# Kernel optimization log

Measured on AMD Instinct MI355X. Metric: run time of the kernel, lower is better.

The kernel has to match this reference:

```python
import jax, jax.numpy as jnp
import numpy as np

S = 4          # num_residual_streams
B = 4          # batch
T = 4096       # seq_len
D = 1024       # dim
SINKHORN_ITERS = 20
EPS = 1e-05


def setup_inputs() -> dict:
    key = jax.random.key(0)
    k1, k2 = jax.random.split(key)
    residuals = jax.random.normal(k1, (B * S, T, D), dtype=jnp.float32)
    rmsnorm_weight = jnp.ones((D,), dtype=jnp.float32)
    # H_pre: -8 everywhere except layer_index % S = 0 -> 0.0
    H_pre_logits = jnp.full((S,), -8.0, dtype=jnp.float32).at[0].set(0.0)
    H_post_logits = jnp.zeros((S,), dtype=jnp.float32)
    # H_res: -8 off-diagonal, 0 on diagonal, plus alpha_init * noise
    H_res = (jnp.full((S, S), -8.0, dtype=jnp.float32) + 8.0 * jnp.eye(S, dtype=jnp.float32)
             + 0.01 * jax.random.normal(k2, (S, S), dtype=jnp.float32))
    return dict(residuals=residuals, rmsnorm_weight=rmsnorm_weight,
                H_pre_logits=H_pre_logits, H_post_logits=H_post_logits, H_res=H_res)


def _sinkhorn_knopp(M, num_iters, eps):
    # alternating row / column normalization to a doubly-stochastic matrix
    for _ in range(num_iters):
        M = M / (M.sum(axis=1, keepdims=True) + eps)
        M = M / (M.sum(axis=0, keepdims=True) + eps)
    return M


def reference(residuals, rmsnorm_weight, H_pre_logits, H_post_logits, H_res):
    s = H_pre_logits.shape[0]
    bs, t, d = residuals.shape
    b = bs // s
    # rearrange '(b s) t d -> (b t) s d'
    x = residuals.reshape(b, s, t, d).transpose(0, 2, 1, 3).reshape(b * t, s, d)
    # stream_aggregate with h_pre = sigmoid(H_pre_logits)
    h_pre = jax.nn.sigmoid(H_pre_logits)
    x_agg = jnp.einsum('nsd,s->nd', x, h_pre)
    # rmsnorm
    rms = jnp.sqrt(jnp.mean(x_agg * x_agg, axis=-1, keepdims=True) + EPS)
    x_norm = (x_agg / rms) * rmsnorm_weight
    # identity branch on the aggregated single-stream view
    branch_out = x_norm  # [(b t), d]
    # stream_distribute with h_post = 2 * sigmoid(H_post_logits)
    h_post = 2.0 * jax.nn.sigmoid(H_post_logits)
    y_dist = branch_out[:, None, :] * h_post[None, :, None]  # [(b t), s, d]
    # stream_mix with sinkhorn-normalized exp(H_res)
    M = _sinkhorn_knopp(jnp.exp(H_res), SINKHORN_ITERS, EPS)
    mixed = jnp.einsum('sr,nrd->nsd', M, y_dist)
    out = x + mixed
    # rearrange '(b t) s d -> (b s) t d'
    out = out.reshape(b, t, s, d).transpose(0, 2, 1, 3).reshape(b * s, t, d)
    return out
```

## Files before the change

kernel.cpp:

```cpp
#include <hip/hip_runtime.h>


#define S_ 4
#define T_ 4096
#define D_ 1024
#define NITER_ 20
#define EPSF_ 1e-5f

__global__ __launch_bounds__(256) void hyperconn_kernel(
    const float* __restrict__ res,
    const float* __restrict__ w,
    const float* __restrict__ hpre_l,
    const float* __restrict__ hpost_l,
    const float* __restrict__ hres,
    float* __restrict__ out)
{
    const int n   = blockIdx.x;
    const int b   = n >> 12;
    const int t   = n & (T_ - 1);
    const int tid = threadIdx.x;

    __shared__ float s_c[S_];
    __shared__ float s_part[4];

    if (tid == 0) {
        float M[S_][S_];
        #pragma unroll
        for (int i = 0; i < S_; ++i)
            #pragma unroll
            for (int j = 0; j < S_; ++j)
                M[i][j] = __expf(hres[i * S_ + j]);
        for (int it = 0; it < NITER_; ++it) {
            #pragma unroll
            for (int i = 0; i < S_; ++i) {
                float srow = M[i][0] + M[i][1] + M[i][2] + M[i][3];
                float inv  = 1.0f / (srow + EPSF_);
                M[i][0] *= inv; M[i][1] *= inv; M[i][2] *= inv; M[i][3] *= inv;
            }
            #pragma unroll
            for (int j = 0; j < S_; ++j) {
                float scol = M[0][j] + M[1][j] + M[2][j] + M[3][j];
                float inv  = 1.0f / (scol + EPSF_);
                M[0][j] *= inv; M[1][j] *= inv; M[2][j] *= inv; M[3][j] *= inv;
            }
        }
        #pragma unroll
        for (int s = 0; s < S_; ++s) {
            float c = 0.0f;
            #pragma unroll
            for (int r = 0; r < S_; ++r) {
                float hp = 2.0f / (1.0f + __expf(-hpost_l[r]));
                c += M[s][r] * hp;
            }
            s_c[s] = c;
        }
    }

    float hpre[S_];
    #pragma unroll
    for (int s = 0; s < S_; ++s)
        hpre[s] = 1.0f / (1.0f + __expf(-hpre_l[s]));

    const float4* res4 = reinterpret_cast<const float4*>(res);
    const float4* w4   = reinterpret_cast<const float4*>(w);
    float4*       out4 = reinterpret_cast<float4*>(out);

    const int    D4      = D_ / 4;
    const size_t rowbase = (size_t)(b * S_) * T_ + t;

    float4 r[S_];
    #pragma unroll
    for (int s = 0; s < S_; ++s)
        r[s] = res4[(rowbase + (size_t)s * T_) * D4 + tid];

    float4 agg;
    agg.x = hpre[0]*r[0].x + hpre[1]*r[1].x + hpre[2]*r[2].x + hpre[3]*r[3].x;
    agg.y = hpre[0]*r[0].y + hpre[1]*r[1].y + hpre[2]*r[2].y + hpre[3]*r[3].y;
    agg.z = hpre[0]*r[0].z + hpre[1]*r[1].z + hpre[2]*r[2].z + hpre[3]*r[3].z;
    agg.w = hpre[0]*r[0].w + hpre[1]*r[1].w + hpre[2]*r[2].w + hpre[3]*r[3].w;

    float ssq = agg.x*agg.x + agg.y*agg.y + agg.z*agg.z + agg.w*agg.w;
    #pragma unroll
    for (int off = 32; off >= 1; off >>= 1)
        ssq += __shfl_down(ssq, off, 64);
    const int lane = tid & 63;
    const int wv   = tid >> 6;
    if (lane == 0) s_part[wv] = ssq;
    __syncthreads();
    const float tot     = s_part[0] + s_part[1] + s_part[2] + s_part[3];
    const float inv_rms = rsqrtf(tot * (1.0f / (float)D_) + EPSF_);

    const float4 wt = w4[tid];
    float4 nrm;
    nrm.x = agg.x * inv_rms * wt.x;
    nrm.y = agg.y * inv_rms * wt.y;
    nrm.z = agg.z * inv_rms * wt.z;
    nrm.w = agg.w * inv_rms * wt.w;

    #pragma unroll
    for (int s = 0; s < S_; ++s) {
        const float c = s_c[s];
        float4 o;
        o.x = r[s].x + nrm.x * c;
        o.y = r[s].y + nrm.y * c;
        o.z = r[s].z + nrm.z * c;
        o.w = r[s].w + nrm.w * c;
        out4[(rowbase + (size_t)s * T_) * D4 + tid] = o;
    }
}

extern "C" void kernel_launch(void* const* d_in, const int* in_sizes, int n_in,
                              void* d_out, int out_size, void* d_ws, size_t ws_size,
                              hipStream_t stream) {
    const float* res     = (const float*)d_in[0];
    const float* weight  = (const float*)d_in[1];
    const float* hpre_l  = (const float*)d_in[2];
    const float* hpost_l = (const float*)d_in[3];
    const float* hres    = (const float*)d_in[4];
    float*       out     = (float*)d_out;

    const int n_rows = in_sizes[0] / (S_ * D_);
    hyperconn_kernel<<<n_rows, 256, 0, stream>>>(res, weight, hpre_l, hpost_l, hres, out);
}
```

Before: 465.9 us.

## Precompute Sinkhorn coefficients in separate kernel and use nontemporal loads/stores

```diff
diff --git a/kernel.cpp b/kernel.cpp
--- a/kernel.cpp
+++ b/kernel.cpp
@@ -7,12 +7,50 @@
 #define NITER_ 20
 #define EPSF_ 1e-5f
 
-__global__ __launch_bounds__(256) void hyperconn_kernel(
+typedef float f32x4 __attribute__((ext_vector_type(4)));
+
+__device__ float g_coef[8];
+
+__global__ void hyperconn_coeff(const float* __restrict__ hpre_l,
+                                const float* __restrict__ hpost_l,
+                                const float* __restrict__ hres)
+{
+    if (threadIdx.x != 0) return;
+
+    float M[S_][S_];
+    #pragma unroll
+    for (int i = 0; i < S_; ++i)
+        #pragma unroll
+        for (int j = 0; j < S_; ++j)
+            M[i][j] = __expf(hres[i * S_ + j]);
+
+    for (int it = 0; it < NITER_; ++it) {
+        #pragma unroll
+        for (int i = 0; i < S_; ++i) {
+            float inv = 1.0f / (M[i][0] + M[i][1] + M[i][2] + M[i][3] + EPSF_);
+            M[i][0] *= inv; M[i][1] *= inv; M[i][2] *= inv; M[i][3] *= inv;
+        }
+        #pragma unroll
+        for (int j = 0; j < S_; ++j) {
+            float inv = 1.0f / (M[0][j] + M[1][j] + M[2][j] + M[3][j] + EPSF_);
+            M[0][j] *= inv; M[1][j] *= inv; M[2][j] *= inv; M[3][j] *= inv;
+        }
+    }
+
+    #pragma unroll
+    for (int s = 0; s < S_; ++s) {
+        g_coef[s] = 1.0f / (1.0f + __expf(-hpre_l[s]));
+        float c = 0.0f;
+        #pragma unroll
+        for (int r = 0; r < S_; ++r)
+            c += M[s][r] * (2.0f / (1.0f + __expf(-hpost_l[r])));
+        g_coef[S_ + s] = c;
+    }
+}
+
+__global__ __launch_bounds__(256) void hyperconn_main(
     const float* __restrict__ res,
     const float* __restrict__ w,
-    const float* __restrict__ hpre_l,
-    const float* __restrict__ hpost_l,
-    const float* __restrict__ hres,
     float* __restrict__ out)
 {
     const int n   = blockIdx.x;
@@ -20,64 +58,26 @@
     const int t   = n & (T_ - 1);
     const int tid = threadIdx.x;
 
-    __shared__ float s_c[S_];
     __shared__ float s_part[4];
 
-    if (tid == 0) {
-        float M[S_][S_];
-        #pragma unroll
-        for (int i = 0; i < S_; ++i)
-            #pragma unroll
-            for (int j = 0; j < S_; ++j)
-                M[i][j] = __expf(hres[i * S_ + j]);
-        for (int it = 0; it < NITER_; ++it) {
-            #pragma unroll
-            for (int i = 0; i < S_; ++i) {
-                float srow = M[i][0] + M[i][1] + M[i][2] + M[i][3];
-                float inv  = 1.0f / (srow + EPSF_);
-                M[i][0] *= inv; M[i][1] *= inv; M[i][2] *= inv; M[i][3] *= inv;
-            }
-            #pragma unroll
-            for (int j = 0; j < S_; ++j) {
-                float scol = M[0][j] + M[1][j] + M[2][j] + M[3][j];
-                float inv  = 1.0f / (scol + EPSF_);
-                M[0][j] *= inv; M[1][j] *= inv; M[2][j] *= inv; M[3][j] *= inv;
-            }
-        }
-        #pragma unroll
-        for (int s = 0; s < S_; ++s) {
-            float c = 0.0f;
-            #pragma unroll
-            for (int r = 0; r < S_; ++r) {
-                float hp = 2.0f / (1.0f + __expf(-hpost_l[r]));
-                c += M[s][r] * hp;
-            }
-            s_c[s] = c;
-        }
-    }
+    const float h0 = g_coef[0], h1 = g_coef[1], h2 = g_coef[2], h3 = g_coef[3];
+    const float c0 = g_coef[4], c1 = g_coef[5], c2 = g_coef[6], c3 = g_coef[7];
 
-    float hpre[S_];
-    #pragma unroll
-    for (int s = 0; s < S_; ++s)
-        hpre[s] = 1.0f / (1.0f + __expf(-hpre_l[s]));
-
-    const float4* res4 = reinterpret_cast<const float4*>(res);
-    const float4* w4   = reinterpret_cast<const float4*>(w);
-    float4*       out4 = reinterpret_cast<float4*>(out);
+    const f32x4* res4 = reinterpret_cast<const f32x4*>(res);
+    const f32x4* w4   = reinterpret_cast<const f32x4*>(w);
+    f32x4*       out4 = reinterpret_cast<f32x4*>(out);
 
     const int    D4      = D_ / 4;
     const size_t rowbase = (size_t)(b * S_) * T_ + t;
+    const size_t sstride = (size_t)T_ * D4;
 
-    float4 r[S_];
+    const size_t base = rowbase * D4 + tid;
+    f32x4 r[S_];
     #pragma unroll
     for (int s = 0; s < S_; ++s)
-        r[s] = res4[(rowbase + (size_t)s * T_) * D4 + tid];
+        r[s] = __builtin_nontemporal_load(&res4[base + (size_t)s * sstride]);
 
-    float4 agg;
-    agg.x = hpre[0]*r[0].x + hpre[1]*r[1].x + hpre[2]*r[2].x + hpre[3]*r[3].x;
-    agg.y = hpre[0]*r[0].y + hpre[1]*r[1].y + hpre[2]*r[2].y + hpre[3]*r[3].y;
-    agg.z = hpre[0]*r[0].z + hpre[1]*r[1].z + hpre[2]*r[2].z + hpre[3]*r[3].z;
-    agg.w = hpre[0]*r[0].w + hpre[1]*r[1].w + hpre[2]*r[2].w + hpre[3]*r[3].w;
+    f32x4 agg = h0 * r[0] + h1 * r[1] + h2 * r[2] + h3 * r[3];
 
     float ssq = agg.x*agg.x + agg.y*agg.y + agg.z*agg.z + agg.w*agg.w;
     #pragma unroll
@@ -90,22 +90,14 @@
     const float tot     = s_part[0] + s_part[1] + s_part[2] + s_part[3];
     const float inv_rms = rsqrtf(tot * (1.0f / (float)D_) + EPSF_);
 
-    const float4 wt = w4[tid];
-    float4 nrm;
-    nrm.x = agg.x * inv_rms * wt.x;
-    nrm.y = agg.y * inv_rms * wt.y;
-    nrm.z = agg.z * inv_rms * wt.z;
-    nrm.w = agg.w * inv_rms * wt.w;
+    const f32x4 wt  = w4[tid];
+    const f32x4 nrm = agg * inv_rms * wt;
 
+    const float cs[S_] = {c0, c1, c2, c3};
     #pragma unroll
     for (int s = 0; s < S_; ++s) {
-        const float c = s_c[s];
-        float4 o;
-        o.x = r[s].x + nrm.x * c;
-        o.y = r[s].y + nrm.y * c;
-        o.z = r[s].z + nrm.z * c;
-        o.w = r[s].w + nrm.w * c;
-        out4[(rowbase + (size_t)s * T_) * D4 + tid] = o;
+        f32x4 o = r[s] + nrm * cs[s];
+        __builtin_nontemporal_store(o, &out4[base + (size_t)s * sstride]);
     }
 }
 
@@ -119,6 +111,8 @@
     const float* hres    = (const float*)d_in[4];
     float*       out     = (float*)d_out;
 
+    hyperconn_coeff<<<1, 64, 0, stream>>>(hpre_l, hpost_l, hres);
+
     const int n_rows = in_sizes[0] / (S_ * D_);
-    hyperconn_kernel<<<n_rows, 256, 0, stream>>>(res, weight, hpre_l, hpost_l, hres, out);
+    hyperconn_main<<<n_rows, 256, 0, stream>>>(res, weight, out);
 }
```

New measurement: 456.3 us. -2.1%, faster.
